# Optimization experiments

Measured on AMD Instinct MI355X. Metric: run time of the kernel, lower is better.

The kernel has to match this reference:

```python
import jax, jax.numpy as jnp
import numpy as np

T, D, H, N = 2048, 2048, 32, 64
DW, DA, DV, DG = 64, 64, 32, 128


def _ln(x, w, b, eps):
    mu = x.mean(-1, keepdims=True)
    var = ((x - mu) ** 2).mean(-1, keepdims=True)
    return (x - mu) * jax.lax.rsqrt(var + eps) * w + b


def setup_inputs() -> dict:
    key = jax.random.key(0)
    ks = iter(jax.random.split(key, 40))

    def rn(shape, s=0.02):
        return jax.random.normal(next(ks), shape, dtype=jnp.float32) * s

    def ru(shape):
        return jax.random.uniform(next(ks), shape, dtype=jnp.float32)

    return dict(
        x=rn((T, D), 1.0),
        state1=rn((1, D), 1.0),
        state2=rn((H, N, N), 0.1),
        v_first=rn((T, D), 1.0),
        ln1_w=jnp.ones((D,), jnp.float32),
        ln1_b=jnp.zeros((D,), jnp.float32),
        x_r=ru((D,)), x_w=ru((D,)), x_k=ru((D,)),
        x_v=ru((D,)), x_a=ru((D,)), x_g=ru((D,)),
        W_r=rn((D, D)), W_k=rn((D, D)), W_v=rn((D, D)), W_o=rn((D, D)),
        w1=rn((D, DW)), w2=rn((DW, D)), w0=rn((D,), 0.5),
        a1=rn((D, DA)), a2=rn((DA, D)), a0=rn((D,), 0.5),
        v1=rn((D, DV)), v2=rn((DV, D)), v0=rn((D,), 0.5),
        g1=rn((D, DG)), g2=rn((DG, D)),
        k_k=rn((D,), 0.5), k_a=rn((D,), 0.5), r_k=rn((D,), 0.5),
        ln_x_w=jnp.ones((D,), jnp.float32),
        ln_x_b=jnp.zeros((D,), jnp.float32),
    )


def reference(x, state1, state2, v_first, ln1_w, ln1_b,
              x_r, x_w, x_k, x_v, x_a, x_g,
              W_r, W_k, W_v, W_o,
              w1, w2, w0, a1, a2, a0, v1, v2, v0, g1, g2,
              k_k, k_a, r_k, ln_x_w, ln_x_b):
    # ln1 + token shift
    xn = _ln(x, ln1_w, ln1_b, 1e-5)                      # [T, D]
    sx = jnp.concatenate([state1, xn[:-1]], axis=0) - xn  # shifted - x
    xr = xn + sx * x_r
    xw = xn + sx * x_w
    xk = xn + sx * x_k
    xv = xn + sx * x_v
    xa = xn + sx * x_a
    xg = xn + sx * x_g

    r = xr @ W_r.T
    # decay: w = exp(-0.606531 * sigmoid(w0 + tanh(xw@w1)@w2))
    w = jnp.exp(-0.606531 * jax.nn.sigmoid(jnp.tanh(xw @ w1) @ w2 + w0))
    k = xk @ W_k.T
    v = xv @ W_v.T
    a = jax.nn.sigmoid(xa @ a1 @ a2 + a0)
    g = jax.nn.sigmoid(xg @ g1) @ g2
    # layer_id != 0: blend with v_first via v-lora
    v = v + (v_first - v) * jax.nn.sigmoid(xv @ v1 @ v2 + v0)

    kh = (k * k_k).reshape(T, H, N)
    kk = kh / (jnp.linalg.norm(kh, axis=-1, keepdims=True) + 1e-6)  # l2norm per head
    k = k * (1.0 + (a - 1.0) * k_a)

    rh = r.reshape(T, H, N)
    wh = w.reshape(T, H, N)
    khh = k.reshape(T, H, N)
    vh = v.reshape(T, H, N)
    ab = kk * a.reshape(T, H, N)  # b input to wkv

    def step(S, t):
        r_t, w_t, k_t, v_t, kk_t, ab_t = t
        sa = jnp.einsum('hij,hj->hi', S, -kk_t)  # state @ a (a = -kk column)
        S = (S * w_t[:, None, :]
             + sa[:, :, None] * ab_t[:, None, :]
             + v_t[:, :, None] * k_t[:, None, :])
        return S, jnp.einsum('hij,hj->hi', S, r_t)

    state2_out, xo = jax.lax.scan(step, state2, (rh, wh, khh, vh, kk, ab))  # xo: [T,H,N]

    # per-head layernorm (ln_x, eps=0.00064), then full-width affine
    xo = _ln(xo, jnp.float32(1.0), jnp.float32(0.0), 0.00064)
    xo = xo.reshape(T, D) * ln_x_w + ln_x_b
    # r_k bonus term
    bonus = ((rh * khh * r_k.reshape(H, N)).sum(-1, keepdims=True) * vh).reshape(T, D)
    xo = (xo + bonus) * g
    out = x + xo @ W_o.T
    return out, xn[-1:], state2_out
```

## Files before the change

kernel.cpp:

```cpp
#include <hip/hip_runtime.h>

#define Tn 2048
#define Dn 2048
#define Hn 32
#define Cn 32
#define NCH (Tn / Cn)

typedef float f32x4 __attribute__((ext_vector_type(4)));
typedef __bf16 bf16x8 __attribute__((ext_vector_type(8)));
typedef __bf16 bf16x4 __attribute__((ext_vector_type(4)));

template <int CTRL>
__device__ __forceinline__ float dpp_add(float x) {
  int xi = __builtin_bit_cast(int, x);
  int sh = __builtin_amdgcn_update_dpp(0, xi, CTRL, 0xf, 0xf, true);
  return x + __builtin_bit_cast(float, sh);
}
__device__ __forceinline__ float rdlane(float x, int l) {
  int xi = __builtin_bit_cast(int, x);
  return __builtin_bit_cast(float, __builtin_amdgcn_readlane(xi, l));
}
__device__ __forceinline__ float waveSum(float v) {
  v = dpp_add<0x111>(v);
  v = dpp_add<0x112>(v);
  v = dpp_add<0x114>(v);
  v = dpp_add<0x118>(v);
  return (rdlane(v, 15) + rdlane(v, 31)) + (rdlane(v, 47) + rdlane(v, 63));
}

__device__ __forceinline__ float sigm(float x) { return 1.f / (1.f + expf(-x)); }

__device__ __forceinline__ void gl_lds16(const void* g, void* l) {
  __builtin_amdgcn_global_load_lds(
      (__attribute__((address_space(1))) void*)(g),
      (__attribute__((address_space(3))) void*)(l), 16, 0, 0);
}

__device__ __forceinline__ void bar_lgkm() {
  asm volatile("s_waitcnt lgkmcnt(0)" ::: "memory");
  __builtin_amdgcn_s_barrier();
}

__device__ __forceinline__ f32x4 mfma16(const __bf16* a, const __bf16* b, f32x4 acc) {
  return __builtin_amdgcn_mfma_f32_16x16x32_bf16(
      *(const bf16x8*)a, *(const bf16x8*)b, acc, 0, 0, 0);
}


__global__ __launch_bounds__(256) void castw3_kernel(
    const float* __restrict__ A, const float* __restrict__ B,
    const float* __restrict__ C, __bf16* __restrict__ o0,
    __bf16* __restrict__ o1, __bf16* __restrict__ o2) {
  const int z = blockIdx.y;
  const float* src = z == 0 ? A : (z == 1 ? B : C);
  __bf16* dst = z == 0 ? o0 : (z == 1 ? o1 : o2);
  const size_t i4 = (size_t)blockIdx.x * 256 + threadIdx.x;
  f32x4 v = *(const f32x4*)(src + i4 * 4);
  bf16x4 o;
  o[0] = (__bf16)v[0]; o[1] = (__bf16)v[1]; o[2] = (__bf16)v[2]; o[3] = (__bf16)v[3];
  ((bf16x4*)dst)[i4] = o;
}

__global__ __launch_bounds__(256) void cast1_kernel(
    const float* __restrict__ src, __bf16* __restrict__ dst) {
  const size_t i4 = (size_t)blockIdx.x * 256 + threadIdx.x;
  f32x4 v = *(const f32x4*)(src + i4 * 4);
  bf16x4 o;
  o[0] = (__bf16)v[0]; o[1] = (__bf16)v[1]; o[2] = (__bf16)v[2]; o[3] = (__bf16)v[3];
  ((bf16x4*)dst)[i4] = o;
}

__global__ __launch_bounds__(256) void castTU_kernel(
    const float* __restrict__ w2, const float* __restrict__ a2,
    const float* __restrict__ v2, const float* __restrict__ g2,
    __bf16* __restrict__ w2T, __bf16* __restrict__ a2T,
    __bf16* __restrict__ v2T, __bf16* __restrict__ g2T,
    const float* __restrict__ w1, const float* __restrict__ a1,
    const float* __restrict__ v1, const float* __restrict__ g1,
    __bf16* __restrict__ uwT, __bf16* __restrict__ uaT,
    __bf16* __restrict__ uvT, __bf16* __restrict__ ugT) {
  const int k = threadIdx.x;
  if (k >= 128) return;
  const int y = blockIdx.y;
  if (y == 0) {
    const int i = blockIdx.x;
    w2T[(size_t)i * 128 + k] = (k < 64) ? (__bf16)w2[(size_t)k * Dn + i] : (__bf16)0.f;
    a2T[(size_t)i * 128 + k] = (k < 64) ? (__bf16)a2[(size_t)k * Dn + i] : (__bf16)0.f;
    v2T[(size_t)i * 128 + k] = (k < 32) ? (__bf16)v2[(size_t)k * Dn + i] : (__bf16)0.f;
    g2T[(size_t)i * 128 + k] = (__bf16)g2[(size_t)k * Dn + i];
  } else {
    const int z = y - 1;
    const float* src = z == 0 ? w1 : (z == 1 ? a1 : (z == 2 ? v1 : g1));
    __bf16* dst = z == 0 ? uwT : (z == 1 ? uaT : (z == 2 ? uvT : ugT));
    const int R = z == 0 ? 64 : (z == 1 ? 64 : (z == 2 ? 32 : 128));
    const int d = blockIdx.x;
    dst[(size_t)k * Dn + d] = (k < R) ? (__bf16)src[(size_t)d * R + k] : (__bf16)0.f;
  }
}


__global__ __launch_bounds__(256) void lnmix_kernel(
    const float* __restrict__ x, const float* __restrict__ state1,
    const float* __restrict__ lw, const float* __restrict__ lb,
    const float* __restrict__ cr, const float* __restrict__ cw,
    const float* __restrict__ ck, const float* __restrict__ cv,
    const float* __restrict__ ca, const float* __restrict__ cg,
    __bf16* __restrict__ br, __bf16* __restrict__ bw, __bf16* __restrict__ bk,
    __bf16* __restrict__ bv, __bf16* __restrict__ ba, __bf16* __restrict__ bg,
    float* __restrict__ xn_last) {
  __shared__ float red[16];
  const int t = blockIdx.x, tid = threadIdx.x;
  const int lane = tid & 63, wv = tid >> 6;
  const float* xc = x + (size_t)t * Dn;
  const float* xp = x + (size_t)(t - 1) * Dn;
  float vc[8], vp[8];
  float sc = 0.f, sp = 0.f;
#pragma unroll
  for (int c = 0; c < 8; ++c) {
    vc[c] = xc[tid + c * 256]; sc += vc[c];
    vp[c] = (t > 0) ? xp[tid + c * 256] : 0.f; sp += vp[c];
  }
  sc = waveSum(sc); sp = waveSum(sp);
  if (lane == 0) { red[wv] = sc; red[8 + wv] = sp; }
  __syncthreads();
  const float mu_c = (red[0] + red[1] + red[2] + red[3]) * (1.f / (float)Dn);
  const float mu_p = (red[8] + red[9] + red[10] + red[11]) * (1.f / (float)Dn);
  float qc = 0.f, qp = 0.f;
#pragma unroll
  for (int c = 0; c < 8; ++c) {
    float d0 = vc[c] - mu_c; qc += d0 * d0;
    float d1 = vp[c] - mu_p; qp += d1 * d1;
  }
  qc = waveSum(qc); qp = waveSum(qp);
  if (lane == 0) { red[4 + wv] = qc; red[12 + wv] = qp; }
  __syncthreads();
  const float var_c = (red[4] + red[5] + red[6] + red[7]) * (1.f / (float)Dn);
  const float var_p = (red[12] + red[13] + red[14] + red[15]) * (1.f / (float)Dn);
  const float rstd_c = rsqrtf(var_c + 1e-5f);
  const float rstd_p = rsqrtf(var_p + 1e-5f);
#pragma unroll
  for (int c = 0; c < 8; ++c) {
    const int d = tid + c * 256;
    const size_t idx = (size_t)t * Dn + d;
    const float lwd = lw[d], lbd = lb[d];
    const float ync = (vc[c] - mu_c) * rstd_c * lwd + lbd;
    const float ynp = (t > 0) ? ((vp[c] - mu_p) * rstd_p * lwd + lbd) : state1[d];
    const float sx = ynp - ync;
    br[idx] = (__bf16)(ync + sx * cr[d]);
    bw[idx] = (__bf16)(ync + sx * cw[d]);
    bk[idx] = (__bf16)(ync + sx * ck[d]);
    bv[idx] = (__bf16)(ync + sx * cv[d]);
    ba[idx] = (__bf16)(ync + sx * ca[d]);
    bg[idx] = (__bf16)(ync + sx * cg[d]);
    if (t == Tn - 1) xn_last[d] = ync;
  }
}


__device__ __forceinline__ void gemm_tile(const __bf16* __restrict__ A,
                                          const __bf16* __restrict__ B,
                                          int K, int row0, int col0,
                                          f32x4 (&acc)[4][4]) {
  __shared__ __attribute__((aligned(16))) __bf16 As[8192];
  __shared__ __attribute__((aligned(16))) __bf16 Bs[8192];
  const int tid = threadIdx.x;
  const int lane = tid & 63, wid = tid >> 6;
  const int wm = (wid >> 1) * 64, wn = (wid & 1) * 64;
  const int lr = lane & 15, lg = lane >> 4;
  for (int kt = 0; kt < K; kt += 64) {
#pragma unroll
    for (int it = 0; it < 4; ++it) {
      const int L = it * 256 + tid;
      const int rr = L >> 3;
      const int usw = (L & 7) ^ (rr & 7);
      const int lb = (it * 256 + wid * 64) * 8;
      gl_lds16(A + (size_t)(row0 + rr) * K + (kt + usw * 8), &As[lb]);
      gl_lds16(B + (size_t)(col0 + rr) * K + (kt + usw * 8), &Bs[lb]);
    }
    __syncthreads();
#pragma unroll
    for (int ks = 0; ks < 2; ++ks) {
      bf16x8 af[4], bfv[4];
#pragma unroll
      for (int mf = 0; mf < 4; ++mf) {
        const int r = wm + mf * 16 + lr;
        af[mf] = *(const bf16x8*)&As[r * 64 + (((ks * 4 + lg) ^ (lr & 7)) * 8)];
      }
#pragma unroll
      for (int nf = 0; nf < 4; ++nf) {
        const int r = wn + nf * 16 + lr;
        bfv[nf] = *(const bf16x8*)&Bs[r * 64 + (((ks * 4 + lg) ^ (lr & 7)) * 8)];
      }
#pragma unroll
      for (int mf = 0; mf < 4; ++mf)
#pragma unroll
        for (int nf = 0; nf < 4; ++nf)
          acc[mf][nf] = __builtin_amdgcn_mfma_f32_16x16x32_bf16(
              af[mf], bfv[nf], acc[mf][nf], 0, 0, 0);
    }
    __syncthreads();
  }
}

__device__ __forceinline__ void xcd_swz16(int& bx, int& by) {
  const int lid = bx + (by << 4);
  const int xcd = lid & 7, idx = lid >> 3;
  bx = ((xcd & 3) << 2) + (idx & 3);
  by = ((xcd >> 2) << 3) + (idx >> 2);
}

__global__ __launch_bounds__(256) void gemm37_kernel(
    const __bf16* __restrict__ A0, const __bf16* __restrict__ A1,
    const __bf16* __restrict__ A2, const __bf16* __restrict__ B0,
    const __bf16* __restrict__ B1, const __bf16* __restrict__ B2,
    __bf16* __restrict__ C0, __bf16* __restrict__ C1, __bf16* __restrict__ C2,
    const __bf16* __restrict__ Aw, const __bf16* __restrict__ Aa,
    const __bf16* __restrict__ Av, const __bf16* __restrict__ Ag,
    const __bf16* __restrict__ Bw, const __bf16* __restrict__ Ba,
    const __bf16* __restrict__ Bv, const __bf16* __restrict__ Bg,
    __bf16* __restrict__ Cw, __bf16* __restrict__ Ca,
    __bf16* __restrict__ Cv, __bf16* __restrict__ Cg) {
  const int z = blockIdx.z;
  if (z >= 3 && blockIdx.y != 0) return;
  const __bf16* A; const __bf16* B; __bf16* C;
  switch (z) {
    case 0: A = A0; B = B0; C = C0; break;
    case 1: A = A1; B = B1; C = C1; break;
    case 2: A = A2; B = B2; C = C2; break;
    case 3: A = Aw; B = Bw; C = Cw; break;
    case 4: A = Aa; B = Ba; C = Ca; break;
    case 5: A = Av; B = Bv; C = Cv; break;
    default: A = Ag; B = Bg; C = Cg; break;
  }
  int bx = blockIdx.x, by = blockIdx.y;
  if (z < 3) xcd_swz16(bx, by);
  const int row0 = bx * 128, col0 = (z < 3) ? by * 128 : 0;
  const int ldc = (z < 3) ? Dn : 128;
  f32x4 acc[4][4] = {};
  gemm_tile(A, B, Dn, row0, col0, acc);
  const int lane = threadIdx.x & 63, wid = threadIdx.x >> 6;
  const int wm = (wid >> 1) * 64, wn = (wid & 1) * 64;
#pragma unroll
  for (int mf = 0; mf < 4; ++mf) {
    const int r0 = row0 + wm + mf * 16 + ((lane >> 4) << 2);
#pragma unroll
    for (int nf = 0; nf < 4; ++nf) {
      const int c0 = col0 + wn + nf * 16 + (lane & 15);
#pragma unroll
      for (int rg = 0; rg < 4; ++rg) {
        float val = acc[mf][nf][rg];
        if (z == 3)      val = tanhf(val);
        else if (z == 6) val = sigm(val);
        C[(size_t)(r0 + rg) * ldc + c0] = (__bf16)val;
      }
    }
  }
}

__global__ __launch_bounds__(256) void gemm_s2_kernel(
    const __bf16* __restrict__ Aw, const __bf16* __restrict__ Aa,
    const __bf16* __restrict__ Av, const __bf16* __restrict__ Ag,
    const __bf16* __restrict__ Bw, const __bf16* __restrict__ Ba,
    const __bf16* __restrict__ Bv, const __bf16* __restrict__ Bg,
    const float* __restrict__ w0, const float* __restrict__ a0,
    const float* __restrict__ v0, __bf16* __restrict__ Cw,
    __bf16* __restrict__ Ca, __bf16* __restrict__ Cv, __bf16* __restrict__ Cg) {
  const int z = blockIdx.z;
  const __bf16* A = z == 0 ? Aw : (z == 1 ? Aa : (z == 2 ? Av : Ag));
  const __bf16* B = z == 0 ? Bw : (z == 1 ? Ba : (z == 2 ? Bv : Bg));
  const float* bias = z == 0 ? w0 : (z == 1 ? a0 : (z == 2 ? v0 : (const float*)0));
  __bf16* C = z == 0 ? Cw : (z == 1 ? Ca : (z == 2 ? Cv : Cg));
  const int row0 = blockIdx.x * 128, col0 = blockIdx.y * 128;
  f32x4 acc[4][4] = {};
  gemm_tile(A, B, 128, row0, col0, acc);
  const int lane = threadIdx.x & 63, wid = threadIdx.x >> 6;
  const int wm = (wid >> 1) * 64, wn = (wid & 1) * 64;
#pragma unroll
  for (int mf = 0; mf < 4; ++mf) {
    const int r0 = row0 + wm + mf * 16 + ((lane >> 4) << 2);
#pragma unroll
    for (int nf = 0; nf < 4; ++nf) {
      const int c0 = col0 + wn + nf * 16 + (lane & 15);
#pragma unroll
      for (int rg = 0; rg < 4; ++rg) {
        float val = acc[mf][nf][rg];
        if (z == 0)      val = expf(-0.606531f * sigm(val + bias[c0]));
        else if (z < 3)  val = sigm(val + bias[c0]);
        C[(size_t)(r0 + rg) * Dn + c0] = (__bf16)val;
      }
    }
  }
}

__global__ __launch_bounds__(256) void gemm_wo_kernel(
    const __bf16* __restrict__ A, const __bf16* __restrict__ B,
    const float* __restrict__ xres, float* __restrict__ C) {
  int bx = blockIdx.x, by = blockIdx.y;
  xcd_swz16(bx, by);
  const int row0 = bx * 128, col0 = by * 128;
  f32x4 acc[4][4] = {};
  gemm_tile(A, B, Dn, row0, col0, acc);
  const int lane = threadIdx.x & 63, wid = threadIdx.x >> 6;
  const int wm = (wid >> 1) * 64, wn = (wid & 1) * 64;
#pragma unroll
  for (int mf = 0; mf < 4; ++mf) {
    const int r0 = row0 + wm + mf * 16 + ((lane >> 4) << 2);
#pragma unroll
    for (int nf = 0; nf < 4; ++nf) {
      const int c0 = col0 + wn + nf * 16 + (lane & 15);
#pragma unroll
      for (int rg = 0; rg < 4; ++rg)
        C[(size_t)(r0 + rg) * Dn + c0] =
            acc[mf][nf][rg] + xres[(size_t)(r0 + rg) * Dn + c0];
    }
  }
}


__global__ __launch_bounds__(256) void prep_kernel(
    const __bf16* __restrict__ r, __bf16* __restrict__ k, __bf16* __restrict__ v,
    const __bf16* __restrict__ a, const __bf16* __restrict__ vb,
    const float* __restrict__ v_first, const float* __restrict__ k_k,
    const float* __restrict__ k_a, const float* __restrict__ r_k,
    __bf16* __restrict__ kk_out, __bf16* __restrict__ ab_out,
    float* __restrict__ dot_out) {
  const int t = blockIdx.x;
  const int lane = threadIdx.x & 63, wv = threadIdx.x >> 6;
#pragma unroll 1
  for (int c = 0; c < 8; ++c) {
    const int d = c * 256 + wv * 64 + lane;
    const size_t idx = (size_t)t * Dn + d;
    const float kvv = (float)k[idx];
    const float kh = kvv * k_k[d];
    const float nrm = sqrtf(waveSum(kh * kh)) + 1e-6f;
    const float kkv = kh / nrm;
    const float av = (float)a[idx];
    float vv = (float)v[idx];
    vv = vv + (v_first[idx] - vv) * (float)vb[idx];
    const float kfv = kvv * (1.f + (av - 1.f) * k_a[d]);
    const float dt = waveSum((float)r[idx] * kfv * r_k[d]);
    kk_out[idx] = (__bf16)kkv;
    ab_out[idx] = (__bf16)(kkv * av);
    k[idx] = (__bf16)kfv;
    v[idx] = (__bf16)vv;
    if (lane == 0) dot_out[t * Hn + (d >> 6)] = dt;
  }
}


__global__ __launch_bounds__(256) void chunkA_kernel(
    const __bf16* __restrict__ wd, const __bf16* __restrict__ kk,
    const __bf16* __restrict__ ab, const __bf16* __restrict__ kf,
    const __bf16* __restrict__ r,
    __bf16* __restrict__ PAg, __bf16* __restrict__ Rtil,
    __bf16* __restrict__ BhatT, __bf16* __restrict__ KhatT,
    __bf16* __restrict__ PKg,
    __bf16* __restrict__ Gbg, __bf16* __restrict__ Gkg,
    float* __restrict__ WCg) {
  const int c = blockIdx.x, h = blockIdx.y;
  const int tid = threadIdx.x;
  const int lane = tid & 63, wid = tid >> 6;
  const int lr = lane & 15, lg = lane >> 4, lk = lg * 8;
  __shared__ __attribute__((aligned(16))) __bf16 A_l[32][72];
  __shared__ __attribute__((aligned(16))) __bf16 B_l[32][72], K_l[32][72], R_l[32][72];
  __shared__ __attribute__((aligned(16))) __bf16 At_t[64][40];
  __shared__ float W_l[33][64];
  __shared__ __attribute__((aligned(16))) __bf16 Mn[32][40], Mt[32][40], Mkat[32][40];
  __shared__ __attribute__((aligned(16))) __bf16 Pa[32][40], Pb[32][40];
  __shared__ __attribute__((aligned(16))) __bf16 Tn_[32][40], Tt_[32][40];
  __shared__ __attribute__((aligned(16))) __bf16 Un_[32][40], Ut_[32][40];

  const size_t rowbase = (size_t)(c * Cn) * Dn + (size_t)h * 64;
  const int tt = tid >> 3, j0 = (tid & 7) * 8;
  const size_t g = rowbase + (size_t)tt * Dn + j0;
  *(bf16x8*)&A_l[tt][j0] = *(const bf16x8*)(wd + g);
  __syncthreads();
  if (tid < 64) {
    const int j = tid;
    float cur = 1.f;
    W_l[0][j] = 1.f;
    for (int t = 0; t < Cn; ++t) {
      cur *= (float)A_l[t][j];
      W_l[t + 1][j] = cur;
    }
    WCg[((size_t)c * Hn + h) * 64 + j] = cur;
  }
  __syncthreads();
  {
    bf16x8 kkv = *(const bf16x8*)(kk + g);
    bf16x8 abv = *(const bf16x8*)(ab + g);
    bf16x8 kv  = *(const bf16x8*)(kf + g);
    bf16x8 rv  = *(const bf16x8*)(r + g);
    bf16x8 oa, ob, ok, orr;
    const size_t tb = ((size_t)c * Hn + h) * 2048;
#pragma unroll
    for (int e = 0; e < 8; ++e) {
      const int j = j0 + e;
      const float Wexc = W_l[tt][j], Winc = W_l[tt + 1][j], WC = W_l[32][j];
      const float inv = 1.f / Winc;
      const float at = -(float)kkv[e] * Wexc;
      const float bt = (float)abv[e] * inv;
      const float kt = (float)kv[e] * inv;
      const float rt = (float)rv[e] * Winc;
      oa[e] = (__bf16)at; ob[e] = (__bf16)bt; ok[e] = (__bf16)kt;
      orr[e] = (__bf16)rt;
      At_t[j][tt] = (__bf16)at;
      BhatT[tb + (size_t)j * 32 + tt] = (__bf16)(bt * WC);
      KhatT[tb + (size_t)j * 32 + tt] = (__bf16)(kt * WC);
    }
    *(bf16x8*)&A_l[tt][j0] = oa;
    *(bf16x8*)&B_l[tt][j0] = ob;
    *(bf16x8*)&K_l[tt][j0] = ok;
    *(bf16x8*)&R_l[tt][j0] = orr;
    *(bf16x8*)(Rtil + g) = orr;
  }
  __syncthreads();
  const size_t matbase = ((size_t)c * Hn + h) * (Cn * Cn);
  {
    const __bf16 (*Ax)[72] = (wid < 2) ? A_l : R_l;
    const __bf16 (*Bx)[72] = ((wid & 1) == 0) ? B_l : K_l;
#pragma unroll
    for (int tile = 0; tile < 4; ++tile) {
      const int tm = (tile >> 1) * 16, tn = (tile & 1) * 16;
      f32x4 acc = {};
      acc = mfma16(&Ax[tm + lr][lk], &Bx[tn + lr][lk], acc);
      acc = mfma16(&Ax[tm + lr][32 + lk], &Bx[tn + lr][32 + lk], acc);
      const int col = tn + lr;
#pragma unroll
      for (int e = 0; e < 4; ++e) {
        const int row = tm + lg * 4 + e;
        if (wid == 0) {
          const __bf16 v = (__bf16)((col < row) ? acc[e] : 0.f);
          Mn[row][col] = v; Mt[col][row] = v;
        } else if (wid == 1) {
          Mkat[col][row] = (__bf16)((col < row) ? acc[e] : 0.f);
        } else if (wid == 2) {
          Gbg[matbase + row * 32 + col] = (__bf16)((col <= row) ? acc[e] : 0.f);
        } else {
          Gkg[matbase + row * 32 + col] = (__bf16)((col <= row) ? acc[e] : 0.f);
        }
      }
    }
  }
  __syncthreads();
  for (int rep = 0; rep < 4; ++rep) {
    const int id = rep * 256 + tid;
    const int t = id >> 5, ta = id & 31;
    Pa[t][ta] = (__bf16)((float)Mn[t][ta] + (t == ta ? 1.f : 0.f));
  }
  __syncthreads();
  const int tm = (wid >> 1) * 16, tn = (wid & 1) * 16;
  auto sq = [&](__bf16 (*Dn_)[40], __bf16 (*Dt_)[40],
                __bf16 (*Xn)[40], __bf16 (*Xt)[40]) {
    f32x4 acc = {};
    acc = mfma16(&Xn[tm + lr][lk], &Xt[tn + lr][lk], acc);
    const int col = tn + lr;
#pragma unroll
    for (int e = 0; e < 4; ++e) {
      const int row = tm + lg * 4 + e;
      const __bf16 v = (__bf16)acc[e];
      Dn_[row][col] = v; Dt_[col][row] = v;
    }
    __syncthreads();
  };
  auto pup = [&](__bf16 (*Dn_)[40], __bf16 (*Pn)[40], __bf16 (*Tt)[40]) {
    f32x4 acc;
    const int col = tn + lr;
#pragma unroll
    for (int e = 0; e < 4; ++e) acc[e] = (float)Pn[tm + lg * 4 + e][col];
    acc = mfma16(&Pn[tm + lr][lk], &Tt[tn + lr][lk], acc);
#pragma unroll
    for (int e = 0; e < 4; ++e) Dn_[tm + lg * 4 + e][col] = (__bf16)acc[e];
    __syncthreads();
  };
  sq(Tn_, Tt_, Mn, Mt);
  pup(Pb, Pa, Tt_);
  sq(Un_, Ut_, Tn_, Tt_);
  pup(Pa, Pb, Ut_);
  sq(Tn_, Tt_, Un_, Ut_);
  pup(Pb, Pa, Tt_);
  sq(Un_, Ut_, Tn_, Tt_);
  pup(Pa, Pb, Ut_);
  {
    f32x4 acc = {};
    acc = mfma16(&Pa[tm + lr][lk], &Mkat[tn + lr][lk], acc);
    const int col = tn + lr;
#pragma unroll
    for (int e = 0; e < 4; ++e)
      PKg[matbase + (tm + lg * 4 + e) * 32 + col] = (__bf16)acc[e];
  }
#pragma unroll
  for (int half = 0; half < 2; ++half) {
    const int jn = (wid & 1) * 16 + half * 32;
    f32x4 acc = {};
    acc = mfma16(&Pa[tm + lr][lk], &At_t[jn + lr][lk], acc);
    const int col = jn + lr;
#pragma unroll
    for (int e = 0; e < 4; ++e)
      PAg[rowbase + (size_t)(tm + lg * 4 + e) * Dn + col] = (__bf16)acc[e];
  }
}


__global__ __launch_bounds__(256) void vt_kernel(
    const __bf16* __restrict__ vbuf, __bf16* __restrict__ Vt) {
  const int c = blockIdx.x, h = blockIdx.y;
  __shared__ __bf16 tile[32][72];
  const int tid = threadIdx.x;
  {
    const int t = tid >> 3, i0 = (tid & 7) * 8;
    *(bf16x8*)&tile[t][i0] =
        *(const bf16x8*)(vbuf + (size_t)(c * Cn + t) * Dn + h * 64 + i0);
  }
  __syncthreads();
  {
    const int i = tid >> 2, t0 = (tid & 3) * 8;
    bf16x8 o;
#pragma unroll
    for (int e = 0; e < 8; ++e) o[e] = tile[t0 + e][i];
    *(bf16x8*)(Vt + ((size_t)c * Hn + h) * 2048 + (size_t)i * 32 + t0) = o;
  }
}


__global__ __launch_bounds__(256) void chunkB_kernel(
    const __bf16* __restrict__ PAg, const __bf16* __restrict__ Rtil,
    const __bf16* __restrict__ BhatT, const __bf16* __restrict__ KhatT,
    const __bf16* __restrict__ PKg,
    const __bf16* __restrict__ Gbg, const __bf16* __restrict__ Gkg,
    const float* __restrict__ WCg, const __bf16* __restrict__ Vt,
    const float* __restrict__ st_in, __bf16* __restrict__ xo,
    float* __restrict__ st_out) {
  const int b = blockIdx.x;
  const int xcd = b & 7, rest = b >> 3;
  const int h = xcd * 4 + (rest & 3);
  const int io = (rest >> 2) * 32;
  const int tid = threadIdx.x;
  const int lane = tid & 63, wid = tid >> 6;
  const int lr = lane & 15, lg = lane >> 4;
  const int lk = lg * 8;

  __shared__ __attribute__((aligned(16))) float S_l[32][68];
  __shared__ __attribute__((aligned(16))) __bf16 Sb_l[32][72];
  __shared__ __attribute__((aligned(16))) __bf16 PA_l[32][72], R_l[32][72];
  __shared__ __attribute__((aligned(16))) __bf16 BhT_l[64][40], KhT_l[64][40];
  __shared__ __attribute__((aligned(16))) __bf16 Vt_l[32][40];
  __shared__ __attribute__((aligned(16))) __bf16 PK_l[32][40];
  __shared__ __attribute__((aligned(16))) __bf16 Gb_l[32][40], Gk_l[32][40];
  __shared__ __attribute__((aligned(16))) __bf16 SA_l[32][40];
  __shared__ float WC_l[64];

  {
    const int i = tid >> 3, j0 = (tid & 7) * 8;
    const float* src = st_in + (size_t)h * 4096 + (size_t)(io + i) * 64 + j0;
    *(f32x4*)&S_l[i][j0] = *(const f32x4*)src;
    *(f32x4*)&S_l[i][j0 + 4] = *(const f32x4*)(src + 4);
  }

  bf16x8 rPA, rR, rBh, rKh;
  bf16x4 rV, rPK, rGb, rGk;
  float rWC = 0.f;

  auto load_regs = [&](int c) {
    const size_t rb = (size_t)(c * Cn) * Dn + (size_t)h * 64;
    {
      const int t = tid >> 3, j0 = (tid & 7) * 8;
      rPA = *(const bf16x8*)(PAg + rb + (size_t)t * Dn + j0);
      rR  = *(const bf16x8*)(Rtil + rb + (size_t)t * Dn + j0);
    }
    const size_t tb = ((size_t)c * Hn + h) * 2048;
    {
      const int jj = tid >> 2, t0 = (tid & 3) * 8;
      rBh = *(const bf16x8*)(BhatT + tb + (size_t)jj * 32 + t0);
      rKh = *(const bf16x8*)(KhatT + tb + (size_t)jj * 32 + t0);
    }
    {
      const int i = tid >> 3, t0 = (tid & 7) * 4;
      rV = *(const bf16x4*)(Vt + tb + (size_t)(io + i) * 32 + t0);
    }
    const size_t mb = ((size_t)c * Hn + h) * 1024 + (size_t)tid * 4;
    rPK = *(const bf16x4*)(PKg + mb);
    rGb = *(const bf16x4*)(Gbg + mb);
    rGk = *(const bf16x4*)(Gkg + mb);
    if (tid < 64) rWC = WCg[((size_t)c * Hn + h) * 64 + tid];
  };
  auto store_lds = [&]() {
    {
      const int t = tid >> 3, j0 = (tid & 7) * 8;
      *(bf16x8*)&PA_l[t][j0] = rPA;
      *(bf16x8*)&R_l[t][j0] = rR;
    }
    {
      const int jj = tid >> 2, t0 = (tid & 3) * 8;
      *(bf16x8*)&BhT_l[jj][t0] = rBh;
      *(bf16x8*)&KhT_l[jj][t0] = rKh;
    }
    {
      const int i = tid >> 3, t0 = (tid & 7) * 4;
      *(bf16x4*)&Vt_l[i][t0] = rV;
    }
    {
      const int t = tid >> 3, u0 = (tid & 7) * 4;
      *(bf16x4*)&PK_l[t][u0] = rPK;
      *(bf16x4*)&Gb_l[t][u0] = rGb;
      *(bf16x4*)&Gk_l[t][u0] = rGk;
    }
    if (tid < 64) WC_l[tid] = rWC;
  };
  auto sb_refresh = [&]() {
    const int i = tid >> 3, j0 = (tid & 7) * 8;
    bf16x8 o;
#pragma unroll
    for (int e = 0; e < 8; ++e) o[e] = (__bf16)S_l[i][j0 + e];
    *(bf16x8*)&Sb_l[i][j0] = o;
  };

  load_regs(0);
  store_lds();
  sb_refresh();
  bar_lgkm();

  const int tm = (wid >> 1) * 16, tn = (wid & 1) * 16;

#pragma unroll 1
  for (int c = 0; c < NCH; ++c) {
    load_regs(c + 1 < NCH ? c + 1 : c);
    {
      f32x4 acc = {};
      acc = mfma16(&PA_l[tm + lr][lk], &Sb_l[tn + lr][lk], acc);
      acc = mfma16(&PA_l[tm + lr][32 + lk], &Sb_l[tn + lr][32 + lk], acc);
      acc = mfma16(&PK_l[tm + lr][lk], &Vt_l[tn + lr][lk], acc);
      bf16x4 o;
#pragma unroll
      for (int e = 0; e < 4; ++e) o[e] = (__bf16)acc[e];
      *(bf16x4*)&SA_l[tn + lr][tm + lg * 4] = o;
    }
    bar_lgkm();
    {
      f32x4 acc = {};
      acc = mfma16(&Gb_l[tm + lr][lk], &SA_l[tn + lr][lk], acc);
      acc = mfma16(&Gk_l[tm + lr][lk], &Vt_l[tn + lr][lk], acc);
      acc = mfma16(&R_l[tm + lr][lk], &Sb_l[tn + lr][lk], acc);
      acc = mfma16(&R_l[tm + lr][32 + lk], &Sb_l[tn + lr][32 + lk], acc);
      const int ig = h * 64 + io + tn + lr;
#pragma unroll
      for (int e = 0; e < 4; ++e)
        xo[(size_t)(c * Cn + tm + lg * 4 + e) * Dn + ig] = (__bf16)acc[e];
    }
#pragma unroll
    for (int tt2 = 0; tt2 < 2; ++tt2) {
      const int tix = wid + tt2 * 4;
      const int im = (tix & 1) * 16, jn = (tix >> 1) * 16;
      const float wc = WC_l[jn + lr];
      f32x4 acc;
#pragma unroll
      for (int e = 0; e < 4; ++e) acc[e] = S_l[im + lg * 4 + e][jn + lr] * wc;
      acc = mfma16(&SA_l[im + lr][lk], &BhT_l[jn + lr][lk], acc);
      acc = mfma16(&Vt_l[im + lr][lk], &KhT_l[jn + lr][lk], acc);
#pragma unroll
      for (int e = 0; e < 4; ++e) S_l[im + lg * 4 + e][jn + lr] = acc[e];
    }
    bar_lgkm();
    store_lds();
    sb_refresh();
    bar_lgkm();
  }
  {
    const int i = tid >> 3, j0 = (tid & 7) * 8;
    float* dst = st_out + (size_t)h * 4096 + (size_t)(io + i) * 64 + j0;
    *(f32x4*)dst = *(const f32x4*)&S_l[i][j0];
    *(f32x4*)(dst + 4) = *(const f32x4*)&S_l[i][j0 + 4];
  }
}


__global__ __launch_bounds__(256) void post_kernel(
    const __bf16* __restrict__ xo, const __bf16* __restrict__ v,
    const __bf16* __restrict__ g, const float* __restrict__ dot,
    const float* __restrict__ lnw, const float* __restrict__ lnb,
    __bf16* __restrict__ out) {
  const int t = blockIdx.x;
  const int lane = threadIdx.x & 63, wv = threadIdx.x >> 6;
#pragma unroll 1
  for (int c = 0; c < 8; ++c) {
    const int d = c * 256 + wv * 64 + lane;
    const size_t idx = (size_t)t * Dn + d;
    const float val = (float)xo[idx];
    const float mu = waveSum(val) * (1.f / 64.f);
    const float ctr = val - mu;
    const float var = waveSum(ctr * ctr) * (1.f / 64.f);
    float y = ctr * rsqrtf(var + 0.00064f);
    y = y * lnw[d] + lnb[d];
    const float res = (y + dot[t * Hn + (d >> 6)] * (float)v[idx]) * (float)g[idx];
    out[idx] = (__bf16)res;
  }
}


extern "C" void kernel_launch(void* const* d_in, const int* in_sizes, int n_in,
                              void* d_out, int out_size, void* d_ws, size_t ws_size,
                              hipStream_t stream) {
  (void)in_sizes; (void)n_in; (void)out_size; (void)ws_size;
  const float* x       = (const float*)d_in[0];
  const float* state1  = (const float*)d_in[1];
  const float* state2  = (const float*)d_in[2];
  const float* v_first = (const float*)d_in[3];
  const float* ln1_w   = (const float*)d_in[4];
  const float* ln1_b   = (const float*)d_in[5];
  const float* x_r     = (const float*)d_in[6];
  const float* x_w     = (const float*)d_in[7];
  const float* x_k     = (const float*)d_in[8];
  const float* x_v     = (const float*)d_in[9];
  const float* x_a     = (const float*)d_in[10];
  const float* x_g     = (const float*)d_in[11];
  const float* W_r     = (const float*)d_in[12];
  const float* W_k     = (const float*)d_in[13];
  const float* W_v     = (const float*)d_in[14];
  const float* W_o     = (const float*)d_in[15];
  const float* w1      = (const float*)d_in[16];
  const float* w2      = (const float*)d_in[17];
  const float* w0      = (const float*)d_in[18];
  const float* a1      = (const float*)d_in[19];
  const float* a2      = (const float*)d_in[20];
  const float* a0      = (const float*)d_in[21];
  const float* v1      = (const float*)d_in[22];
  const float* v2      = (const float*)d_in[23];
  const float* v0      = (const float*)d_in[24];
  const float* g1      = (const float*)d_in[25];
  const float* g2      = (const float*)d_in[26];
  const float* k_k     = (const float*)d_in[27];
  const float* k_a     = (const float*)d_in[28];
  const float* r_k     = (const float*)d_in[29];
  const float* lnx_w   = (const float*)d_in[30];
  const float* lnx_b   = (const float*)d_in[31];

  char* p = (char*)d_ws;
  const size_t MB = 1ull << 20;
  __bf16* PAg   = (__bf16*)(p + 0 * MB);
  __bf16* xr_b  = (__bf16*)(p + 8 * MB);
  __bf16* Wo_b  = (__bf16*)(p + 8 * MB);
  __bf16* xw_b  = (__bf16*)(p + 16 * MB);
  __bf16* wdec  = (__bf16*)(p + 16 * MB);
  __bf16* xo_b  = (__bf16*)(p + 16 * MB);
  __bf16* xk_b  = (__bf16*)(p + 24 * MB);
  __bf16* abuf  = (__bf16*)(p + 24 * MB);
  __bf16* Rtil  = (__bf16*)(p + 24 * MB);
  __bf16* xv_b  = (__bf16*)(p + 32 * MB);
  __bf16* vbl   = (__bf16*)(p + 32 * MB);
  __bf16* BhatT = (__bf16*)(p + 32 * MB);
  __bf16* xa_b  = (__bf16*)(p + 40 * MB);
  __bf16* gbuf  = (__bf16*)(p + 40 * MB);
  __bf16* xg_b  = (__bf16*)(p + 48 * MB);
  __bf16* kkbuf = (__bf16*)(p + 48 * MB);
  __bf16* xobuf = (__bf16*)(p + 48 * MB);
  __bf16* Wr_b  = (__bf16*)(p + 56 * MB);
  __bf16* abbuf = (__bf16*)(p + 56 * MB);
  __bf16* Wk_b  = (__bf16*)(p + 64 * MB);
  __bf16* KhatT = (__bf16*)(p + 64 * MB);
  __bf16* Wv_b  = (__bf16*)(p + 72 * MB);
  __bf16* PKg   = (__bf16*)(p + 72 * MB);
  __bf16* rbuf  = (__bf16*)(p + 80 * MB);
  __bf16* kbuf  = (__bf16*)(p + 88 * MB);
  __bf16* Vt    = (__bf16*)(p + 88 * MB);
  __bf16* vbuf  = (__bf16*)(p + 96 * MB);
  __bf16* Gbg   = (__bf16*)(p + 104 * MB);
  __bf16* Gkg   = (__bf16*)(p + 108 * MB);
  char* q = p + 112 * MB;
  __bf16* yw  = (__bf16*)q; q += (size_t)Tn * 128 * 2;
  __bf16* ya  = (__bf16*)q; q += (size_t)Tn * 128 * 2;
  __bf16* yv  = (__bf16*)q; q += (size_t)Tn * 128 * 2;
  __bf16* yg  = (__bf16*)q; q += (size_t)Tn * 128 * 2;
  __bf16* uwT = (__bf16*)q; q += (size_t)128 * Dn * 2;
  __bf16* uaT = (__bf16*)q; q += (size_t)128 * Dn * 2;
  __bf16* uvT = (__bf16*)q; q += (size_t)128 * Dn * 2;
  __bf16* ugT = (__bf16*)q; q += (size_t)128 * Dn * 2;
  __bf16* w2T = (__bf16*)q; q += (size_t)Dn * 128 * 2;
  __bf16* a2T = (__bf16*)q; q += (size_t)Dn * 128 * 2;
  __bf16* v2T = (__bf16*)q; q += (size_t)Dn * 128 * 2;
  __bf16* g2T = (__bf16*)q; q += (size_t)Dn * 128 * 2;
  float*  dot = (float*)q;  q += (size_t)Tn * Hn * 4;
  float*  WCg = (float*)q;  q += (size_t)NCH * Hn * 64 * 4;

  float* out     = (float*)d_out;
  float* out_xnl = out + (size_t)Tn * Dn;
  float* out_st  = out_xnl + Dn;

  castw3_kernel<<<dim3(4096, 3), 256, 0, stream>>>(W_r, W_k, W_v, Wr_b, Wk_b, Wv_b);
  castTU_kernel<<<dim3(2048, 5), 256, 0, stream>>>(
      w2, a2, v2, g2, w2T, a2T, v2T, g2T,
      w1, a1, v1, g1, uwT, uaT, uvT, ugT);
  lnmix_kernel<<<2048, 256, 0, stream>>>(
      x, state1, ln1_w, ln1_b, x_r, x_w, x_k, x_v, x_a, x_g,
      xr_b, xw_b, xk_b, xv_b, xa_b, xg_b, out_xnl);
  gemm37_kernel<<<dim3(16, 16, 7), 256, 0, stream>>>(
      xr_b, xk_b, xv_b, Wr_b, Wk_b, Wv_b, rbuf, kbuf, vbuf,
      xw_b, xa_b, xv_b, xg_b, uwT, uaT, uvT, ugT, yw, ya, yv, yg);
  cast1_kernel<<<4096, 256, 0, stream>>>(W_o, Wo_b);
  gemm_s2_kernel<<<dim3(16, 16, 4), 256, 0, stream>>>(
      yw, ya, yv, yg, w2T, a2T, v2T, g2T, w0, a0, v0, wdec, abuf, vbl, gbuf);
  prep_kernel<<<2048, 256, 0, stream>>>(rbuf, kbuf, vbuf, abuf, vbl, v_first,
                                        k_k, k_a, r_k, kkbuf, abbuf, dot);
  chunkA_kernel<<<dim3(NCH, Hn), 256, 0, stream>>>(
      wdec, kkbuf, abbuf, kbuf, rbuf,
      PAg, Rtil, BhatT, KhatT, PKg, Gbg, Gkg, WCg);
  vt_kernel<<<dim3(NCH, Hn), 256, 0, stream>>>(vbuf, Vt);
  chunkB_kernel<<<64, 256, 0, stream>>>(
      PAg, Rtil, BhatT, KhatT, PKg, Gbg, Gkg, WCg, Vt,
      state2, xobuf, out_st);
  post_kernel<<<2048, 256, 0, stream>>>(xobuf, vbuf, gbuf, dot, lnx_w, lnx_b, xo_b);
  gemm_wo_kernel<<<dim3(16, 16), 256, 0, stream>>>(xo_b, Wo_b, x, out);
}
```

Baseline: 350.7 us.

## Double-buffer chunk LDS tiles and write bf16 state copy inline

Per-chunk operand tiles in LDS (PA, R, Bh, Kh, V, PK, Gb, Gk, WC) are now double-buffered, so the next chunk's registers are stored into the other buffer right after the state update. This removes one of the three barriers per chunk. The bf16 state mirror is now written directly from the MFMA accumulators instead of a separate refresh pass that re-read the fp32 state. The cost is roughly double the LDS footprint, which could reduce occupancy.

```diff
diff --git a/kernel.cpp b/kernel.cpp
--- a/kernel.cpp
+++ b/kernel.cpp
@@ -541,14 +541,14 @@
   const int lk = lg * 8;
 
   __shared__ __attribute__((aligned(16))) float S_l[32][68];
-  __shared__ __attribute__((aligned(16))) __bf16 Sb_l[32][72];
-  __shared__ __attribute__((aligned(16))) __bf16 PA_l[32][72], R_l[32][72];
-  __shared__ __attribute__((aligned(16))) __bf16 BhT_l[64][40], KhT_l[64][40];
-  __shared__ __attribute__((aligned(16))) __bf16 Vt_l[32][40];
-  __shared__ __attribute__((aligned(16))) __bf16 PK_l[32][40];
-  __shared__ __attribute__((aligned(16))) __bf16 Gb_l[32][40], Gk_l[32][40];
+  __shared__ __attribute__((aligned(16))) __bf16 Sb_l[2][32][72];
+  __shared__ __attribute__((aligned(16))) __bf16 PA_l[2][32][72], R_l[2][32][72];
+  __shared__ __attribute__((aligned(16))) __bf16 BhT_l[2][64][40], KhT_l[2][64][40];
+  __shared__ __attribute__((aligned(16))) __bf16 Vt_l[2][32][40];
+  __shared__ __attribute__((aligned(16))) __bf16 PK_l[2][32][40];
+  __shared__ __attribute__((aligned(16))) __bf16 Gb_l[2][32][40], Gk_l[2][32][40];
   __shared__ __attribute__((aligned(16))) __bf16 SA_l[32][40];
-  __shared__ float WC_l[64];
+  __shared__ float WC_l[2][64];
 
   {
     const int i = tid >> 3, j0 = (tid & 7) * 8;
@@ -584,52 +584,52 @@
     rGk = *(const bf16x4*)(Gkg + mb);
     if (tid < 64) rWC = WCg[((size_t)c * Hn + h) * 64 + tid];
   };
-  auto store_lds = [&]() {
+  auto store_lds = [&](int buf) {
     {
       const int t = tid >> 3, j0 = (tid & 7) * 8;
-      *(bf16x8*)&PA_l[t][j0] = rPA;
-      *(bf16x8*)&R_l[t][j0] = rR;
+      *(bf16x8*)&PA_l[buf][t][j0] = rPA;
+      *(bf16x8*)&R_l[buf][t][j0] = rR;
     }
     {
       const int jj = tid >> 2, t0 = (tid & 3) * 8;
-      *(bf16x8*)&BhT_l[jj][t0] = rBh;
-      *(bf16x8*)&KhT_l[jj][t0] = rKh;
+      *(bf16x8*)&BhT_l[buf][jj][t0] = rBh;
+      *(bf16x8*)&KhT_l[buf][jj][t0] = rKh;
     }
     {
       const int i = tid >> 3, t0 = (tid & 7) * 4;
-      *(bf16x4*)&Vt_l[i][t0] = rV;
+      *(bf16x4*)&Vt_l[buf][i][t0] = rV;
     }
     {
       const int t = tid >> 3, u0 = (tid & 7) * 4;
-      *(bf16x4*)&PK_l[t][u0] = rPK;
-      *(bf16x4*)&Gb_l[t][u0] = rGb;
-      *(bf16x4*)&Gk_l[t][u0] = rGk;
-    }
-    if (tid < 64) WC_l[tid] = rWC;
+      *(bf16x4*)&PK_l[buf][t][u0] = rPK;
+      *(bf16x4*)&Gb_l[buf][t][u0] = rGb;
+      *(bf16x4*)&Gk_l[buf][t][u0] = rGk;
+    }
+    if (tid < 64) WC_l[buf][tid] = rWC;
   };
-  auto sb_refresh = [&]() {
+
+  load_regs(0);
+  store_lds(0);
+  {
     const int i = tid >> 3, j0 = (tid & 7) * 8;
     bf16x8 o;
 #pragma unroll
     for (int e = 0; e < 8; ++e) o[e] = (__bf16)S_l[i][j0 + e];
-    *(bf16x8*)&Sb_l[i][j0] = o;
-  };
-
-  load_regs(0);
-  store_lds();
-  sb_refresh();
+    *(bf16x8*)&Sb_l[0][i][j0] = o;
+  }
   bar_lgkm();
 
   const int tm = (wid >> 1) * 16, tn = (wid & 1) * 16;
 
 #pragma unroll 1
   for (int c = 0; c < NCH; ++c) {
+    const int cur = c & 1, nxt = cur ^ 1;
     load_regs(c + 1 < NCH ? c + 1 : c);
     {
       f32x4 acc = {};
-      acc = mfma16(&PA_l[tm + lr][lk], &Sb_l[tn + lr][lk], acc);
-      acc = mfma16(&PA_l[tm + lr][32 + lk], &Sb_l[tn + lr][32 + lk], acc);
-      acc = mfma16(&PK_l[tm + lr][lk], &Vt_l[tn + lr][lk], acc);
+      acc = mfma16(&PA_l[cur][tm + lr][lk], &Sb_l[cur][tn + lr][lk], acc);
+      acc = mfma16(&PA_l[cur][tm + lr][32 + lk], &Sb_l[cur][tn + lr][32 + lk], acc);
+      acc = mfma16(&PK_l[cur][tm + lr][lk], &Vt_l[cur][tn + lr][lk], acc);
       bf16x4 o;
 #pragma unroll
       for (int e = 0; e < 4; ++e) o[e] = (__bf16)acc[e];
@@ -638,10 +638,10 @@
     bar_lgkm();
     {
       f32x4 acc = {};
-      acc = mfma16(&Gb_l[tm + lr][lk], &SA_l[tn + lr][lk], acc);
-      acc = mfma16(&Gk_l[tm + lr][lk], &Vt_l[tn + lr][lk], acc);
-      acc = mfma16(&R_l[tm + lr][lk], &Sb_l[tn + lr][lk], acc);
-      acc = mfma16(&R_l[tm + lr][32 + lk], &Sb_l[tn + lr][32 + lk], acc);
+      acc = mfma16(&Gb_l[cur][tm + lr][lk], &SA_l[tn + lr][lk], acc);
+      acc = mfma16(&Gk_l[cur][tm + lr][lk], &Vt_l[cur][tn + lr][lk], acc);
+      acc = mfma16(&R_l[cur][tm + lr][lk], &Sb_l[cur][tn + lr][lk], acc);
+      acc = mfma16(&R_l[cur][tm + lr][32 + lk], &Sb_l[cur][tn + lr][32 + lk], acc);
       const int ig = h * 64 + io + tn + lr;
 #pragma unroll
       for (int e = 0; e < 4; ++e)
@@ -651,18 +651,19 @@
     for (int tt2 = 0; tt2 < 2; ++tt2) {
       const int tix = wid + tt2 * 4;
       const int im = (tix & 1) * 16, jn = (tix >> 1) * 16;
-      const float wc = WC_l[jn + lr];
+      const float wc = WC_l[cur][jn + lr];
       f32x4 acc;
 #pragma unroll
       for (int e = 0; e < 4; ++e) acc[e] = S_l[im + lg * 4 + e][jn + lr] * wc;
-      acc = mfma16(&SA_l[im + lr][lk], &BhT_l[jn + lr][lk], acc);
-      acc = mfma16(&Vt_l[im + lr][lk], &KhT_l[jn + lr][lk], acc);
-#pragma unroll
-      for (int e = 0; e < 4; ++e) S_l[im + lg * 4 + e][jn + lr] = acc[e];
-    }
-    bar_lgkm();
-    store_lds();
-    sb_refresh();
+      acc = mfma16(&SA_l[im + lr][lk], &BhT_l[cur][jn + lr][lk], acc);
+      acc = mfma16(&Vt_l[cur][im + lr][lk], &KhT_l[cur][jn + lr][lk], acc);
+#pragma unroll
+      for (int e = 0; e < 4; ++e) {
+        S_l[im + lg * 4 + e][jn + lr] = acc[e];
+        Sb_l[nxt][im + lg * 4 + e][jn + lr] = (__bf16)acc[e];
+      }
+    }
+    store_lds(nxt);
     bar_lgkm();
   }
   {
```

Result: no change. 355.0 us (+1.2%).
